# Kernel tuning notes

Measured on AMD Instinct MI355X. Metric: run time of the kernel, lower is better.

The kernel has to match this reference:

```python
import jax, jax.numpy as jnp
import numpy as np

N_NODES = 40000


def _gcn_conv(x, edge_index, W, b):
    """PyG GCNConv: add self-loops, symmetric degree normalization,
    linear transform, gather-scale-scatter aggregation, bias."""
    n = x.shape[0]
    loops = jnp.arange(n, dtype=edge_index.dtype)
    src = jnp.concatenate([edge_index[0], loops])  # [E+N]
    dst = jnp.concatenate([edge_index[1], loops])  # [E+N]
    ones = jnp.ones(src.shape[0], dtype=x.dtype)
    deg = jax.ops.segment_sum(ones, dst, num_segments=n)  # in-degree incl. self-loop
    dinv = jnp.where(deg > 0, jax.lax.rsqrt(deg), 0.0)
    norm = dinv[src] * dinv[dst]  # [E+N]
    h = x @ W  # [n, out]
    msg = h[src] * norm[:, None]  # [E+N, out] gather + scale
    out = jax.ops.segment_sum(msg, dst, num_segments=n)  # scatter-add
    return out + b


def setup_inputs() -> dict:
    key = jax.random.key(0)
    k = jax.random.split(key, 6)
    n, din, dh, dout = N_NODES, 128, 128, 64
    x = jax.random.normal(k[0], (n, din), dtype=jnp.float32)
    edge_index = jax.random.randint(k[1], (2, 640000), 0, n, dtype=jnp.int64)
    W1 = jax.random.normal(k[2], (din, dh), dtype=jnp.float32) / np.sqrt(din)
    b1 = jnp.zeros((dh,), dtype=jnp.float32)
    W2 = jax.random.normal(k[3], (dh, dout), dtype=jnp.float32) / np.sqrt(dh)
    b2 = jnp.zeros((dout,), dtype=jnp.float32)
    return {"x": x, "edge_index": edge_index, "W1": W1, "b1": b1, "W2": W2, "b2": b2}


def reference(x, edge_index, W1, b1, W2, b2):
    h = jax.nn.relu(_gcn_conv(x, edge_index, W1, b1))
    return _gcn_conv(h, edge_index, W2, b2)
```

## Files before the change

kernel.cpp:

```cpp
#include <hip/hip_runtime.h>
#include <hip/hip_fp16.h>


#define N_NODES 40000
#define DIN 128
#define DH 128
#define DOUT 64
#define NEDGES 640000
#define CAP 64
#define NBUCKET 640
#define I4_PER_CHUNK 2000
#define NODES_PER_XCD 5000

typedef _Float16 f16x8 __attribute__((ext_vector_type(8)));
typedef float f32x4 __attribute__((ext_vector_type(4)));

__global__ void k_init(int* __restrict__ deg, const float* __restrict__ W1,
                       const float* __restrict__ W2,
                       _Float16* __restrict__ WT1, _Float16* __restrict__ WT2, int n) {
    int i = blockIdx.x * 256 + threadIdx.x;
    if (i < n) deg[i] = 0;
    if (i < DIN * DH) {
        int k = i >> 7, nn = i & 127;
        WT1[(size_t)nn * DIN + k] = (_Float16)W1[i];
    }
    if (i < DH * DOUT) {
        int k = i >> 6, nn = i & 63;
        WT2[(size_t)nn * DH + k] = (_Float16)W2[i];
    }
}

__global__ __launch_bounds__(256) void k_work1(
    const float* __restrict__ x, const _Float16* __restrict__ WT,
    __half* __restrict__ h,
    const int4* __restrict__ src4, const int4* __restrict__ dst4,
    int* __restrict__ deg, unsigned short* __restrict__ ssrc)
{
    if (blockIdx.x < NBUCKET) {
        const int xg = blockIdx.x & 7;
        const int c  = blockIdx.x >> 3;
        const int lo = xg * NODES_PER_XCD, hi = lo + NODES_PER_XCD;
        const int e0 = c * I4_PER_CHUNK, e1 = e0 + I4_PER_CHUNK;
        for (int e = e0 + threadIdx.x; e < e1; e += 256) {
            int4 d = dst4[e];
            int4 s = src4[e];
            if (d.x >= lo && d.x < hi) {
                int p = atomicAdd(&deg[d.x], 1);
                if (p < CAP) ssrc[d.x * CAP + p] = (unsigned short)s.x;
            }
            if (d.y >= lo && d.y < hi) {
                int p = atomicAdd(&deg[d.y], 1);
                if (p < CAP) ssrc[d.y * CAP + p] = (unsigned short)s.y;
            }
            if (d.z >= lo && d.z < hi) {
                int p = atomicAdd(&deg[d.z], 1);
                if (p < CAP) ssrc[d.z * CAP + p] = (unsigned short)s.z;
            }
            if (d.w >= lo && d.w < hi) {
                int p = atomicAdd(&deg[d.w], 1);
                if (p < CAP) ssrc[d.w * CAP + p] = (unsigned short)s.w;
            }
        }
    } else {
        const int wave = (blockIdx.x - NBUCKET) * 4 + (threadIdx.x >> 6);
        const int lane = threadIdx.x & 63;
        const int m = lane & 15, quad = lane >> 4;

        f32x4 acc[8];
#pragma unroll
        for (int nt = 0; nt < 8; ++nt) acc[nt] = (f32x4){0.f, 0.f, 0.f, 0.f};

        const float* xrow = x + (size_t)(wave * 16 + m) * DIN + quad * 8;
#pragma unroll
        for (int ks = 0; ks < 4; ++ks) {
            float4 xa = *(const float4*)(xrow + ks * 32);
            float4 xb = *(const float4*)(xrow + ks * 32 + 4);
            f16x8 a = { (_Float16)xa.x, (_Float16)xa.y, (_Float16)xa.z, (_Float16)xa.w,
                        (_Float16)xb.x, (_Float16)xb.y, (_Float16)xb.z, (_Float16)xb.w };
#pragma unroll
            for (int nt = 0; nt < 8; ++nt) {
                f16x8 b = *(const f16x8*)(WT + (size_t)(nt * 16 + m) * DIN + ks * 32 + quad * 8);
                acc[nt] = __builtin_amdgcn_mfma_f32_16x16x32_f16(a, b, acc[nt], 0, 0, 0);
            }
        }
#pragma unroll
        for (int r = 0; r < 4; ++r) {
            int orow = wave * 16 + quad * 4 + r;
#pragma unroll
            for (int nt = 0; nt < 8; ++nt)
                h[(size_t)orow * DH + nt * 16 + m] = (__half)acc[nt][r];
        }
    }
}

__global__ __launch_bounds__(256) void k_agg1g2(
    const int* __restrict__ deg, const unsigned short* __restrict__ ssrc,
    const __half* __restrict__ h1, const float* __restrict__ b1,
    const _Float16* __restrict__ WT2, __half* __restrict__ h2)
{
    __shared__ _Float16 xs[16][136];
    const int w = threadIdx.x >> 6;
    const int lane = threadIdx.x & 63;
    const int node0 = blockIdx.x * 16;
    const __half2* hp = (const __half2*)h1;

    for (int i = 0; i < 4; ++i) {
        const int node = node0 + w * 4 + i;
        const int dg = deg[node];
        const int cnt = min(dg, CAP);
        const float dn = rsqrtf((float)(dg + 1));
        float2 self = __half22float2(hp[(size_t)node * 64 + lane]);
        float2 acc = { self.x * dn, self.y * dn };
        int sv = (lane < cnt) ? (int)ssrc[node * CAP + lane] : 0;
        float dval = (lane < cnt) ? rsqrtf((float)(deg[sv] + 1)) : 0.f;
        int e = 0;
        for (; e + 4 <= cnt; e += 4) {
            int s0 = __shfl(sv, e),     s1 = __shfl(sv, e + 1);
            int s2 = __shfl(sv, e + 2), s3 = __shfl(sv, e + 3);
            float w0 = __shfl(dval, e),     w1 = __shfl(dval, e + 1);
            float w2 = __shfl(dval, e + 2), w3 = __shfl(dval, e + 3);
            float2 v0 = __half22float2(hp[(size_t)s0 * 64 + lane]);
            float2 v1 = __half22float2(hp[(size_t)s1 * 64 + lane]);
            float2 v2 = __half22float2(hp[(size_t)s2 * 64 + lane]);
            float2 v3 = __half22float2(hp[(size_t)s3 * 64 + lane]);
            acc.x += (v0.x * w0 + v1.x * w1) + (v2.x * w2 + v3.x * w3);
            acc.y += (v0.y * w0 + v1.y * w1) + (v2.y * w2 + v3.y * w3);
        }
        for (; e < cnt; ++e) {
            int s = __shfl(sv, e);
            float wv = __shfl(dval, e);
            float2 v = __half22float2(hp[(size_t)s * 64 + lane]);
            acc.x += v.x * wv; acc.y += v.y * wv;
        }
        float vx = dn * acc.x + b1[2 * lane];
        float vy = dn * acc.y + b1[2 * lane + 1];
        xs[w * 4 + i][2 * lane]     = (_Float16)(vx > 0.f ? vx : 0.f);
        xs[w * 4 + i][2 * lane + 1] = (_Float16)(vy > 0.f ? vy : 0.f);
    }
    __syncthreads();

    const int m = lane & 15, quad = lane >> 4;
    f32x4 acc2 = (f32x4){0.f, 0.f, 0.f, 0.f};
#pragma unroll
    for (int ks = 0; ks < 4; ++ks) {
        f16x8 a = *(const f16x8*)&xs[m][ks * 32 + quad * 8];
        f16x8 b = *(const f16x8*)(WT2 + (size_t)(w * 16 + m) * DH + ks * 32 + quad * 8);
        acc2 = __builtin_amdgcn_mfma_f32_16x16x32_f16(a, b, acc2, 0, 0, 0);
    }
#pragma unroll
    for (int r = 0; r < 4; ++r) {
        int nrow = node0 + quad * 4 + r;
        float dn = rsqrtf((float)(deg[nrow] + 1));
        h2[(size_t)nrow * DOUT + w * 16 + m] = (__half)(acc2[r] * dn);
    }
}

__global__ __launch_bounds__(256) void k_agg2(
    const int* __restrict__ deg, const unsigned short* __restrict__ ssrc,
    const __half* __restrict__ h, const float* __restrict__ b2,
    float* __restrict__ out)
{
    const int node = blockIdx.x * 4 + (threadIdx.x >> 6);
    const int lane = threadIdx.x & 63;
    const int dg = deg[node];
    const int cnt = min(dg, CAP);
    float acc = (float)h[(size_t)node * 64 + lane];
    int sv = (lane < cnt) ? (int)ssrc[node * CAP + lane] : 0;
    int e = 0;
    for (; e + 8 <= cnt; e += 8) {
        int s0 = __shfl(sv, e),     s1 = __shfl(sv, e + 1);
        int s2 = __shfl(sv, e + 2), s3 = __shfl(sv, e + 3);
        int s4 = __shfl(sv, e + 4), s5 = __shfl(sv, e + 5);
        int s6 = __shfl(sv, e + 6), s7 = __shfl(sv, e + 7);
        float v0 = (float)h[(size_t)s0 * 64 + lane];
        float v1 = (float)h[(size_t)s1 * 64 + lane];
        float v2 = (float)h[(size_t)s2 * 64 + lane];
        float v3 = (float)h[(size_t)s3 * 64 + lane];
        float v4 = (float)h[(size_t)s4 * 64 + lane];
        float v5 = (float)h[(size_t)s5 * 64 + lane];
        float v6 = (float)h[(size_t)s6 * 64 + lane];
        float v7 = (float)h[(size_t)s7 * 64 + lane];
        acc += ((v0 + v1) + (v2 + v3)) + ((v4 + v5) + (v6 + v7));
    }
    for (; e < cnt; ++e) {
        int s = __shfl(sv, e);
        acc += (float)h[(size_t)s * 64 + lane];
    }
    out[(size_t)node * 64 + lane] = rsqrtf((float)(dg + 1)) * acc + b2[lane];
}

extern "C" void kernel_launch(void* const* d_in, const int* in_sizes, int n_in,
                              void* d_out, int out_size, void* d_ws, size_t ws_size,
                              hipStream_t stream) {
    const float* x  = (const float*)d_in[0];
    const int*   ei = (const int*)d_in[1];
    const float* W1 = (const float*)d_in[2];
    const float* b1 = (const float*)d_in[3];
    const float* W2 = (const float*)d_in[4];
    const float* b2 = (const float*)d_in[5];
    float* out = (float*)d_out;

    const int n = N_NODES, E = NEDGES;
    const int* src = ei;
    const int* dst = ei + E;

    char* ws = (char*)d_ws;
    int*            deg  = (int*)(ws + 0);
    _Float16*       WT1  = (_Float16*)(ws + 163840);
    _Float16*       WT2  = (_Float16*)(ws + 196608);
    unsigned short* ssrc = (unsigned short*)(ws + 212992);
    __half*         h1   = (__half*)(ws + 5332992);
    __half*         h2   = (__half*)(ws + 15572992);

    k_init   <<<(n + 255) / 256, 256, 0, stream>>>(deg, W1, W2, WT1, WT2, n);
    k_work1  <<<NBUCKET + 625, 256, 0, stream>>>(x, WT1, h1, (const int4*)src,
                                                 (const int4*)dst, deg, ssrc);
    k_agg1g2 <<<n / 16, 256, 0, stream>>>(deg, ssrc, h1, b1, WT2, h2);
    k_agg2   <<<n / 4,  256, 0, stream>>>(deg, ssrc, h2, b2, out);
}
```

Before: 172.2 us.

## Split bucketing finer, one wave per node in agg1, half-wave edge split in agg2

The bucket count in the combined edge-bucketing/transform kernel goes up fourfold and the per-chunk size goes down, which spreads scatter work over more blocks. k_agg1g2 now runs 1024-thread blocks with one wave per node instead of four nodes per wave, and its gather loop is unrolled to 8. Only 4 of the 16 waves do the MFMA step. k_agg2 splits each wave into two halves that gather alternate edges as half2 loads, then combines them with a cross-half shuffle. This raises memory-level parallelism, at the cost of larger blocks and idle waves during the MFMA phase.

```diff
diff --git a/kernel.cpp b/kernel.cpp
--- a/kernel.cpp
+++ b/kernel.cpp
@@ -8,8 +8,8 @@
 #define DOUT 64
 #define NEDGES 640000
 #define CAP 64
-#define NBUCKET 640
-#define I4_PER_CHUNK 2000
+#define NBUCKET 2560
+#define I4_PER_CHUNK 500
 #define NODES_PER_XCD 5000
 
 typedef _Float16 f16x8 __attribute__((ext_vector_type(8)));
@@ -93,7 +93,7 @@
     }
 }
 
-__global__ __launch_bounds__(256) void k_agg1g2(
+__global__ __launch_bounds__(1024) void k_agg1g2(
     const int* __restrict__ deg, const unsigned short* __restrict__ ssrc,
     const __half* __restrict__ h1, const float* __restrict__ b1,
     const _Float16* __restrict__ WT2, __half* __restrict__ h2)
@@ -102,56 +102,66 @@
     const int w = threadIdx.x >> 6;
     const int lane = threadIdx.x & 63;
     const int node0 = blockIdx.x * 16;
+    const int node = node0 + w;
     const __half2* hp = (const __half2*)h1;
 
-    for (int i = 0; i < 4; ++i) {
-        const int node = node0 + w * 4 + i;
-        const int dg = deg[node];
-        const int cnt = min(dg, CAP);
-        const float dn = rsqrtf((float)(dg + 1));
-        float2 self = __half22float2(hp[(size_t)node * 64 + lane]);
-        float2 acc = { self.x * dn, self.y * dn };
-        int sv = (lane < cnt) ? (int)ssrc[node * CAP + lane] : 0;
-        float dval = (lane < cnt) ? rsqrtf((float)(deg[sv] + 1)) : 0.f;
-        int e = 0;
-        for (; e + 4 <= cnt; e += 4) {
-            int s0 = __shfl(sv, e),     s1 = __shfl(sv, e + 1);
-            int s2 = __shfl(sv, e + 2), s3 = __shfl(sv, e + 3);
-            float w0 = __shfl(dval, e),     w1 = __shfl(dval, e + 1);
-            float w2 = __shfl(dval, e + 2), w3 = __shfl(dval, e + 3);
-            float2 v0 = __half22float2(hp[(size_t)s0 * 64 + lane]);
-            float2 v1 = __half22float2(hp[(size_t)s1 * 64 + lane]);
-            float2 v2 = __half22float2(hp[(size_t)s2 * 64 + lane]);
-            float2 v3 = __half22float2(hp[(size_t)s3 * 64 + lane]);
-            acc.x += (v0.x * w0 + v1.x * w1) + (v2.x * w2 + v3.x * w3);
-            acc.y += (v0.y * w0 + v1.y * w1) + (v2.y * w2 + v3.y * w3);
-        }
-        for (; e < cnt; ++e) {
-            int s = __shfl(sv, e);
-            float wv = __shfl(dval, e);
-            float2 v = __half22float2(hp[(size_t)s * 64 + lane]);
-            acc.x += v.x * wv; acc.y += v.y * wv;
-        }
-        float vx = dn * acc.x + b1[2 * lane];
-        float vy = dn * acc.y + b1[2 * lane + 1];
-        xs[w * 4 + i][2 * lane]     = (_Float16)(vx > 0.f ? vx : 0.f);
-        xs[w * 4 + i][2 * lane + 1] = (_Float16)(vy > 0.f ? vy : 0.f);
-    }
+    const int dg = deg[node];
+    const int cnt = min(dg, CAP);
+    const float dn = rsqrtf((float)(dg + 1));
+    float2 self = __half22float2(hp[(size_t)node * 64 + lane]);
+    float2 acc = { self.x * dn, self.y * dn };
+    int sv = (lane < cnt) ? (int)ssrc[node * CAP + lane] : 0;
+    float dval = (lane < cnt) ? rsqrtf((float)(deg[sv] + 1)) : 0.f;
+    int e = 0;
+    for (; e + 8 <= cnt; e += 8) {
+        int s0 = __shfl(sv, e),     s1 = __shfl(sv, e + 1);
+        int s2 = __shfl(sv, e + 2), s3 = __shfl(sv, e + 3);
+        int s4 = __shfl(sv, e + 4), s5 = __shfl(sv, e + 5);
+        int s6 = __shfl(sv, e + 6), s7 = __shfl(sv, e + 7);
+        float w0 = __shfl(dval, e),     w1 = __shfl(dval, e + 1);
+        float w2 = __shfl(dval, e + 2), w3 = __shfl(dval, e + 3);
+        float w4 = __shfl(dval, e + 4), w5 = __shfl(dval, e + 5);
+        float w6 = __shfl(dval, e + 6), w7 = __shfl(dval, e + 7);
+        float2 v0 = __half22float2(hp[(size_t)s0 * 64 + lane]);
+        float2 v1 = __half22float2(hp[(size_t)s1 * 64 + lane]);
+        float2 v2 = __half22float2(hp[(size_t)s2 * 64 + lane]);
+        float2 v3 = __half22float2(hp[(size_t)s3 * 64 + lane]);
+        float2 v4 = __half22float2(hp[(size_t)s4 * 64 + lane]);
+        float2 v5 = __half22float2(hp[(size_t)s5 * 64 + lane]);
+        float2 v6 = __half22float2(hp[(size_t)s6 * 64 + lane]);
+        float2 v7 = __half22float2(hp[(size_t)s7 * 64 + lane]);
+        acc.x += (v0.x * w0 + v1.x * w1) + (v2.x * w2 + v3.x * w3)
+               + (v4.x * w4 + v5.x * w5) + (v6.x * w6 + v7.x * w7);
+        acc.y += (v0.y * w0 + v1.y * w1) + (v2.y * w2 + v3.y * w3)
+               + (v4.y * w4 + v5.y * w5) + (v6.y * w6 + v7.y * w7);
+    }
+    for (; e < cnt; ++e) {
+        int s = __shfl(sv, e);
+        float wv = __shfl(dval, e);
+        float2 v = __half22float2(hp[(size_t)s * 64 + lane]);
+        acc.x += v.x * wv; acc.y += v.y * wv;
+    }
+    float vx = dn * acc.x + b1[2 * lane];
+    float vy = dn * acc.y + b1[2 * lane + 1];
+    xs[w][2 * lane]     = (_Float16)(vx > 0.f ? vx : 0.f);
+    xs[w][2 * lane + 1] = (_Float16)(vy > 0.f ? vy : 0.f);
     __syncthreads();
 
-    const int m = lane & 15, quad = lane >> 4;
-    f32x4 acc2 = (f32x4){0.f, 0.f, 0.f, 0.f};
-#pragma unroll
-    for (int ks = 0; ks < 4; ++ks) {
-        f16x8 a = *(const f16x8*)&xs[m][ks * 32 + quad * 8];
-        f16x8 b = *(const f16x8*)(WT2 + (size_t)(w * 16 + m) * DH + ks * 32 + quad * 8);
-        acc2 = __builtin_amdgcn_mfma_f32_16x16x32_f16(a, b, acc2, 0, 0, 0);
-    }
-#pragma unroll
-    for (int r = 0; r < 4; ++r) {
-        int nrow = node0 + quad * 4 + r;
-        float dn = rsqrtf((float)(deg[nrow] + 1));
-        h2[(size_t)nrow * DOUT + w * 16 + m] = (__half)(acc2[r] * dn);
+    if (w < 4) {
+        const int m = lane & 15, quad = lane >> 4;
+        f32x4 acc2 = (f32x4){0.f, 0.f, 0.f, 0.f};
+#pragma unroll
+        for (int ks = 0; ks < 4; ++ks) {
+            f16x8 a = *(const f16x8*)&xs[m][ks * 32 + quad * 8];
+            f16x8 b = *(const f16x8*)(WT2 + (size_t)(w * 16 + m) * DH + ks * 32 + quad * 8);
+            acc2 = __builtin_amdgcn_mfma_f32_16x16x32_f16(a, b, acc2, 0, 0, 0);
+        }
+#pragma unroll
+        for (int r = 0; r < 4; ++r) {
+            int nrow = node0 + quad * 4 + r;
+            float dnr = rsqrtf((float)(deg[nrow] + 1));
+            h2[(size_t)nrow * DOUT + w * 16 + m] = (__half)(acc2[r] * dnr);
+        }
     }
 }
 
@@ -162,31 +172,56 @@
 {
     const int node = blockIdx.x * 4 + (threadIdx.x >> 6);
     const int lane = threadIdx.x & 63;
+    const int half = lane >> 5;
+    const int lp = lane & 31;
     const int dg = deg[node];
     const int cnt = min(dg, CAP);
-    float acc = (float)h[(size_t)node * 64 + lane];
+    const __half2* hp = (const __half2*)h;
+
+    float2 acc;
+    if (half == 0) acc = __half22float2(hp[(size_t)node * 32 + lp]);
+    else           acc = make_float2(0.f, 0.f);
+
     int sv = (lane < cnt) ? (int)ssrc[node * CAP + lane] : 0;
     int e = 0;
-    for (; e + 8 <= cnt; e += 8) {
-        int s0 = __shfl(sv, e),     s1 = __shfl(sv, e + 1);
-        int s2 = __shfl(sv, e + 2), s3 = __shfl(sv, e + 3);
-        int s4 = __shfl(sv, e + 4), s5 = __shfl(sv, e + 5);
-        int s6 = __shfl(sv, e + 6), s7 = __shfl(sv, e + 7);
-        float v0 = (float)h[(size_t)s0 * 64 + lane];
-        float v1 = (float)h[(size_t)s1 * 64 + lane];
-        float v2 = (float)h[(size_t)s2 * 64 + lane];
-        float v3 = (float)h[(size_t)s3 * 64 + lane];
-        float v4 = (float)h[(size_t)s4 * 64 + lane];
-        float v5 = (float)h[(size_t)s5 * 64 + lane];
-        float v6 = (float)h[(size_t)s6 * 64 + lane];
-        float v7 = (float)h[(size_t)s7 * 64 + lane];
-        acc += ((v0 + v1) + (v2 + v3)) + ((v4 + v5) + (v6 + v7));
-    }
-    for (; e < cnt; ++e) {
+    for (; e + 16 <= cnt; e += 16) {
+        int b = e + half;
+        int s0 = __shfl(sv, b),      s1 = __shfl(sv, b + 2);
+        int s2 = __shfl(sv, b + 4),  s3 = __shfl(sv, b + 6);
+        int s4 = __shfl(sv, b + 8),  s5 = __shfl(sv, b + 10);
+        int s6 = __shfl(sv, b + 12), s7 = __shfl(sv, b + 14);
+        float2 v0 = __half22float2(hp[(size_t)s0 * 32 + lp]);
+        float2 v1 = __half22float2(hp[(size_t)s1 * 32 + lp]);
+        float2 v2 = __half22float2(hp[(size_t)s2 * 32 + lp]);
+        float2 v3 = __half22float2(hp[(size_t)s3 * 32 + lp]);
+        float2 v4 = __half22float2(hp[(size_t)s4 * 32 + lp]);
+        float2 v5 = __half22float2(hp[(size_t)s5 * 32 + lp]);
+        float2 v6 = __half22float2(hp[(size_t)s6 * 32 + lp]);
+        float2 v7 = __half22float2(hp[(size_t)s7 * 32 + lp]);
+        acc.x += ((v0.x + v1.x) + (v2.x + v3.x)) + ((v4.x + v5.x) + (v6.x + v7.x));
+        acc.y += ((v0.y + v1.y) + (v2.y + v3.y)) + ((v4.y + v5.y) + (v6.y + v7.y));
+    }
+    for (; e + 2 <= cnt; e += 2) {
+        int s = __shfl(sv, e + half);
+        float2 v = __half22float2(hp[(size_t)s * 32 + lp]);
+        acc.x += v.x; acc.y += v.y;
+    }
+    if (e < cnt) {
         int s = __shfl(sv, e);
-        acc += (float)h[(size_t)s * 64 + lane];
-    }
-    out[(size_t)node * 64 + lane] = rsqrtf((float)(dg + 1)) * acc + b2[lane];
+        if (half == 0) {
+            float2 v = __half22float2(hp[(size_t)s * 32 + lp]);
+            acc.x += v.x; acc.y += v.y;
+        }
+    }
+    acc.x += __shfl_xor(acc.x, 32);
+    acc.y += __shfl_xor(acc.y, 32);
+    if (half == 0) {
+        float dn = rsqrtf((float)(dg + 1));
+        float2 o;
+        o.x = dn * acc.x + b2[2 * lp];
+        o.y = dn * acc.y + b2[2 * lp + 1];
+        *(float2*)&out[(size_t)node * 64 + 2 * lp] = o;
+    }
 }
 
 extern "C" void kernel_launch(void* const* d_in, const int* in_sizes, int n_in,
@@ -215,6 +250,6 @@
     k_init   <<<(n + 255) / 256, 256, 0, stream>>>(deg, W1, W2, WT1, WT2, n);
     k_work1  <<<NBUCKET + 625, 256, 0, stream>>>(x, WT1, h1, (const int4*)src,
                                                  (const int4*)dst, deg, ssrc);
-    k_agg1g2 <<<n / 16, 256, 0, stream>>>(deg, ssrc, h1, b1, WT2, h2);
+    k_agg1g2 <<<n / 16, 1024, 0, stream>>>(deg, ssrc, h1, b1, WT2, h2);
     k_agg2   <<<n / 4,  256, 0, stream>>>(deg, ssrc, h2, b2, out);
 }
```

Measured after the change: 179.3 us. 1.04x slower.
